# Optimization experiments

Measured on AMD Instinct MI355X. Metric: run time of the kernel, lower is better.

Reference implementation:

```python
import jax, jax.numpy as jnp
import numpy as np

N_ATOMS = 100000
N_EDGES = 1600000
N_FRAGS = 10000
N_FRAG_EDGES = 80000
D = 128


def setup_inputs() -> dict:
    key = jax.random.key(0)
    ks = jax.random.split(key, 16)
    s = 1.0 / np.sqrt(D)
    return {
        "x_atoms": jax.random.normal(ks[0], (N_ATOMS, D), jnp.float32),
        "edge_index": jax.random.randint(ks[1], (2, N_EDGES), 0, N_ATOMS),
        "edge_attr": jax.random.normal(ks[2], (N_EDGES, D), jnp.float32),
        "frag_index": jax.random.randint(ks[3], (2, N_FRAG_EDGES), 0, N_FRAGS),
        "x_frags": jax.random.normal(ks[4], (N_FRAGS, D), jnp.float32),
        "atom_to_frag_ids": jax.random.randint(ks[5], (N_ATOMS,), 0, N_FRAGS),
        # parameters (stored [in, out]); only layers actually used in forward
        "atom_w": jax.random.uniform(ks[6], (D, D), jnp.float32, -s, s),
        "atom_b": jax.random.uniform(ks[7], (D,), jnp.float32, -s, s),
        "edge_w": jax.random.uniform(ks[8], (D, D), jnp.float32, -s, s),
        "edge_b": jax.random.uniform(ks[9], (D,), jnp.float32, -s, s),
        "frag_w1": jax.random.uniform(ks[10], (D, 2 * D), jnp.float32, -s, s),
        "frag_b1": jax.random.uniform(ks[11], (2 * D,), jnp.float32, -s, s),
        "frag_w2": jax.random.uniform(ks[12], (2 * D, D), jnp.float32, -(1.0 / np.sqrt(2 * D)), 1.0 / np.sqrt(2 * D)),
        "frag_b2": jax.random.uniform(ks[13], (D,), jnp.float32, -(1.0 / np.sqrt(2 * D)), 1.0 / np.sqrt(2 * D)),
    }


def reference(x_atoms, edge_index, edge_attr, frag_index, x_frags,
              atom_to_frag_ids, atom_w, atom_b, edge_w, edge_b,
              frag_w1, frag_b1, frag_w2, frag_b2):
    n = x_atoms.shape[0]
    n_frags = x_frags.shape[0]

    # add self loops
    loop = jnp.arange(n, dtype=edge_index.dtype)
    src = jnp.concatenate([edge_index[0], loop])
    tgt = jnp.concatenate([edge_index[1], loop])
    self_loop_attr = jnp.zeros((n, edge_attr.shape[1]), edge_attr.dtype)
    edge_attr_full = jnp.concatenate([edge_attr, self_loop_attr], axis=0)

    # embeddings
    h = x_atoms @ atom_w + atom_b                      # [N, D]
    _e = edge_attr_full @ edge_w + edge_b              # computed but unused (as in source)

    # symmetric degree normalization over source-node degree
    deg = jax.ops.segment_sum(jnp.ones_like(src, dtype=h.dtype), src, num_segments=n)
    dinv = jnp.where(deg > 0, deg ** -0.5, 0.0)
    norm = dinv[src] * dinv[tgt]                       # [E+N]

    # gather - scale - scatter_add
    msg = h[src] * norm[:, None]                       # [E+N, D]
    x_atoms_new = jax.ops.segment_sum(msg, tgt, num_segments=n)

    # pool atoms into fragments
    frag_feats = jax.ops.segment_sum(x_atoms_new, atom_to_frag_ids, num_segments=n_frags)

    # fragment-level message passing
    fsrc, ftgt = frag_index[0], frag_index[1]
    frag_sum = jax.ops.segment_sum(frag_feats[fsrc], ftgt, num_segments=n_frags)

    # frag_mlp: Linear(D, 2D) -> ReLU -> Linear(2D, D)
    x_frags_new = jax.nn.relu(frag_sum @ frag_w1 + frag_b1) @ frag_w2 + frag_b2
    return (x_atoms_new, x_frags_new)
```

## Files before the change

### kernel.cpp

```cpp
#include <hip/hip_runtime.h>

constexpr int DD = 128;

typedef __attribute__((ext_vector_type(8))) short short8_t;
typedef __attribute__((ext_vector_type(8))) unsigned short ushort8_t;
typedef __attribute__((ext_vector_type(4))) float f32x4;

__device__ __forceinline__ float bf2f(unsigned short u) {
  union { unsigned int i; float f; } c;
  c.i = ((unsigned int)u) << 16;
  return c.f;
}
__device__ __forceinline__ unsigned short f2bf(float f) {
  union { float f; unsigned int i; } c;
  c.f = f;
  unsigned int x = c.i;
  x += 0x7fff + ((x >> 16) & 1);
  return (unsigned short)(x >> 16);
}

__global__ void __launch_bounds__(256) counts_gemm_k(
    const int* __restrict__ esrc, const int* __restrict__ etgt, int E,
    const int* __restrict__ a2f, int N, const int* __restrict__ ftgt, int FE,
    int* __restrict__ cnt_src, int* __restrict__ cnt_tgt,
    int* __restrict__ cnt_a2f, int* __restrict__ cnt_fe,
    int* __restrict__ rank_tgt, int* __restrict__ rank_a2f, int* __restrict__ rank_fe,
    const float* __restrict__ x, const float* __restrict__ W,
    const float* __restrict__ bias, unsigned short* __restrict__ hout,
    int nb_gemm) {
  __shared__ unsigned int wt[8192];

  if ((int)blockIdx.x >= nb_gemm) {
    int i = ((int)blockIdx.x - nb_gemm) * 256 + threadIdx.x;
    if (i < E) {
      atomicAdd(&cnt_src[esrc[i]], 1);
      rank_tgt[i] = atomicAdd(&cnt_tgt[etgt[i]], 1);
    } else if (i < E + N) {
      int j = i - E;
      rank_a2f[j] = atomicAdd(&cnt_a2f[a2f[j]], 1);
    } else if (i < E + N + FE) {
      int e = i - E - N;
      rank_fe[e] = atomicAdd(&cnt_fe[ftgt[e]], 1);
    }
    return;
  }

  const int tid = threadIdx.x;
  const int rbase = blockIdx.x * 128;

  {
    int c = tid & 127;
    int half = tid >> 7;
#pragma unroll 4
    for (int j = 0; j < 32; j++) {
      int p = j * 2 + half;
      int k = p * 2;
      float w0 = W[k * 128 + c];
      float w1 = W[(k + 1) * 128 + c];
      unsigned int packed = (unsigned int)f2bf(w0) | ((unsigned int)f2bf(w1) << 16);
      wt[(64 * c + p) ^ ((c & 7) << 2)] = packed;
    }
  }

  const int wave = tid >> 6;
  const int lane = tid & 63;
  const int l15 = lane & 15;
  const int kg = lane >> 4;

  float bcol[8];
#pragma unroll
  for (int ct = 0; ct < 8; ct++) bcol[ct] = bias[ct * 16 + l15];

  __syncthreads();

  f32x4 acc[2][8];
#pragma unroll
  for (int rt = 0; rt < 2; rt++)
#pragma unroll
    for (int ct = 0; ct < 8; ct++) acc[rt][ct] = (f32x4)(0.f);

#pragma unroll
  for (int ks = 0; ks < 4; ks++) {
    int kcol = ks * 32 + kg * 8;
    short8_t a[2];
#pragma unroll
    for (int rt = 0; rt < 2; rt++) {
      int row = rbase + wave * 32 + rt * 16 + l15;
      if (row < N) {
        const float4* xr = reinterpret_cast<const float4*>(x + (size_t)row * 128 + kcol);
        float4 v0 = xr[0], v1 = xr[1];
        a[rt][0] = (short)f2bf(v0.x); a[rt][1] = (short)f2bf(v0.y);
        a[rt][2] = (short)f2bf(v0.z); a[rt][3] = (short)f2bf(v0.w);
        a[rt][4] = (short)f2bf(v1.x); a[rt][5] = (short)f2bf(v1.y);
        a[rt][6] = (short)f2bf(v1.z); a[rt][7] = (short)f2bf(v1.w);
      } else {
#pragma unroll
        for (int e = 0; e < 8; e++) a[rt][e] = 0;
      }
    }
#pragma unroll
    for (int ct = 0; ct < 8; ct++) {
      int col = ct * 16 + l15;
      int dw0 = (64 * col + ks * 16 + kg * 4) ^ ((col & 7) << 2);
      short8_t b = *reinterpret_cast<const short8_t*>(&wt[dw0]);
      acc[0][ct] = __builtin_amdgcn_mfma_f32_16x16x32_bf16(a[0], b, acc[0][ct], 0, 0, 0);
      acc[1][ct] = __builtin_amdgcn_mfma_f32_16x16x32_bf16(a[1], b, acc[1][ct], 0, 0, 0);
    }
  }

#pragma unroll
  for (int rt = 0; rt < 2; rt++)
#pragma unroll
    for (int ct = 0; ct < 8; ct++)
#pragma unroll
      for (int i = 0; i < 4; i++) {
        int gr = rbase + wave * 32 + rt * 16 + kg * 4 + i;
        if (gr < N)
          hout[(size_t)gr * 128 + ct * 16 + l15] = f2bf(acc[rt][ct][i] + bcol[ct]);
      }
}

template<int IC, int OC, bool RELU, int RPT>
__global__ void __launch_bounds__(256) linear_k(
    const float* __restrict__ in, const float* __restrict__ W,
    const float* __restrict__ bias, float* __restrict__ out, int nrows) {
  constexpr int GROUPS = 256 / OC;
  constexpr int RBLK = RPT * GROUPS;
  __shared__ float xs[RBLK * IC];
  const int tid = threadIdx.x;
  const int c = tid % OC;
  const int g = tid / OC;
  const int rbase = blockIdx.x * RBLK;

  constexpr int NV = RBLK * IC / 4;
  const float4* in4 = reinterpret_cast<const float4*>(in);
  for (int idx = tid; idx < NV; idx += 256) {
    int r = idx / (IC / 4);
    int kk = idx % (IC / 4);
    int gr = rbase + r;
    float4 v = make_float4(0.f, 0.f, 0.f, 0.f);
    if (gr < nrows) v = in4[(size_t)gr * (IC / 4) + kk];
    reinterpret_cast<float4*>(xs)[idx] = v;
  }
  __syncthreads();

  float acc[RPT];
  float b = bias[c];
#pragma unroll
  for (int m = 0; m < RPT; m++) acc[m] = b;

#pragma unroll 4
  for (int k = 0; k < IC; k++) {
    float w = W[k * OC + c];
#pragma unroll
    for (int m = 0; m < RPT; m++)
      acc[m] += xs[(g + m * GROUPS) * IC + k] * w;
  }

#pragma unroll
  for (int m = 0; m < RPT; m++) {
    int gr = rbase + g + m * GROUPS;
    if (gr < nrows) {
      float v = acc[m];
      if (RELU) v = fmaxf(v, 0.f);
      out[(size_t)gr * OC + c] = v;
    }
  }
}

__global__ void __launch_bounds__(256) scanA_k(
    const int* __restrict__ cnt_tgt, int n, int nb, int* __restrict__ bsums,
    const int* __restrict__ cnt_a2f, int* __restrict__ off_a2f,
    const int* __restrict__ cnt_fe, int* __restrict__ off_fe, int nf) {
  __shared__ int s[256];
  int t = threadIdx.x;
  int bid = blockIdx.x;
  if (bid < nb) {
    int base = bid * 1024;
    int v = 0;
    for (int i = t; i < 1024; i += 256) {
      int g = base + i;
      if (g < n) v += cnt_tgt[g];
    }
    s[t] = v;
    __syncthreads();
    for (int d = 128; d > 0; d >>= 1) {
      if (t < d) s[t] += s[t + d];
      __syncthreads();
    }
    if (t == 0) bsums[bid] = s[0];
  } else {
    const int* in = (bid == nb) ? cnt_a2f : cnt_fe;
    int* off = (bid == nb) ? off_a2f : off_fe;
    int carry = 0;
    for (int base = 0; base < nf; base += 256) {
      int v = (base + t < nf) ? in[base + t] : 0;
      __syncthreads();
      s[t] = v;
      __syncthreads();
      for (int d = 1; d < 256; d <<= 1) {
        int u = (t >= d) ? s[t - d] : 0;
        __syncthreads();
        s[t] += u;
        __syncthreads();
      }
      if (base + t < nf) off[base + t] = s[t] - v + carry;
      carry += s[255];
    }
  }
}

__global__ void __launch_bounds__(256) scanB_k(
    const int* __restrict__ in, int n, const int* __restrict__ bsums,
    int* __restrict__ off, const int* __restrict__ cnt_src,
    float* __restrict__ dinv) {
  __shared__ int s[256];
  int t = threadIdx.x;
  int bid = blockIdx.x;
  s[t] = (t < bid) ? bsums[t] : 0;
  __syncthreads();
  for (int d = 128; d > 0; d >>= 1) {
    if (t < d) s[t] += s[t + d];
    __syncthreads();
  }
  int prefix = s[0];
  __syncthreads();

  int base = bid * 1024 + t * 4;
  int a0 = (base + 0 < n) ? in[base + 0] : 0;
  int a1 = (base + 1 < n) ? in[base + 1] : 0;
  int a2 = (base + 2 < n) ? in[base + 2] : 0;
  int a3 = (base + 3 < n) ? in[base + 3] : 0;
  int tot = a0 + a1 + a2 + a3;
  s[t] = tot;
  __syncthreads();
  for (int d = 1; d < 256; d <<= 1) {
    int u = (t >= d) ? s[t - d] : 0;
    __syncthreads();
    s[t] += u;
    __syncthreads();
  }
  int pre = s[t] - tot + prefix;
  int e0 = pre, e1 = pre + a0, e2 = e1 + a1, e3 = e2 + a2;
  if (base + 0 < n) { off[base + 0] = e0; dinv[base + 0] = rsqrtf((float)(cnt_src[base + 0] + 1)); }
  if (base + 1 < n) { off[base + 1] = e1; dinv[base + 1] = rsqrtf((float)(cnt_src[base + 1] + 1)); }
  if (base + 2 < n) { off[base + 2] = e2; dinv[base + 2] = rsqrtf((float)(cnt_src[base + 2] + 1)); }
  if (base + 3 < n) { off[base + 3] = e3; dinv[base + 3] = rsqrtf((float)(cnt_src[base + 3] + 1)); }
}

__global__ void __launch_bounds__(256) fill_k(
    const int* __restrict__ esrc, const int* __restrict__ etgt, int E,
    const int* __restrict__ a2f, int N,
    const int* __restrict__ fsrc, const int* __restrict__ ftgt, int FE,
    const int* __restrict__ off_tgt, const int* __restrict__ rank_tgt,
    const int* __restrict__ off_a2f, const int* __restrict__ rank_a2f,
    const int* __restrict__ off_fe, const int* __restrict__ rank_fe,
    int* __restrict__ csr_src, int* __restrict__ aids, int* __restrict__ csr_fs) {
  int i = blockIdx.x * 256 + threadIdx.x;
  if (i < E) {
    csr_src[off_tgt[etgt[i]] + rank_tgt[i]] = esrc[i];
  } else if (i < E + N) {
    int j = i - E;
    aids[off_a2f[a2f[j]] + rank_a2f[j]] = j;
  } else if (i < E + N + FE) {
    int e = i - E - N;
    csr_fs[off_fe[ftgt[e]] + rank_fe[e]] = fsrc[e];
  }
}

__global__ void __launch_bounds__(256) edge_gather_k(
    const int* __restrict__ off, const int* __restrict__ cnt,
    const int* __restrict__ csr_src, const unsigned short* __restrict__ h,
    const float* __restrict__ dinv, float* __restrict__ out, int n) {
  int tn = blockIdx.x * 16 + (threadIdx.x >> 4);
  if (tn >= n) return;
  int lane = threadIdx.x & 15;
  const ushort8_t* h8 = reinterpret_cast<const ushort8_t*>(h);
  float dt = dinv[tn];
  ushort8_t hv = h8[(size_t)tn * 16 + lane];
  float acc[8];
#pragma unroll
  for (int e = 0; e < 8; e++) acc[e] = bf2f(hv[e]) * dt;
  int s0 = off[tn], c = cnt[tn];
  int i = 0;
  for (; i + 4 <= c; i += 4) {
    int s1 = csr_src[s0 + i + 0];
    int s2 = csr_src[s0 + i + 1];
    int s3 = csr_src[s0 + i + 2];
    int s4 = csr_src[s0 + i + 3];
    float d1 = dinv[s1], d2 = dinv[s2], d3 = dinv[s3], d4 = dinv[s4];
    ushort8_t v1 = h8[(size_t)s1 * 16 + lane];
    ushort8_t v2 = h8[(size_t)s2 * 16 + lane];
    ushort8_t v3 = h8[(size_t)s3 * 16 + lane];
    ushort8_t v4 = h8[(size_t)s4 * 16 + lane];
#pragma unroll
    for (int e = 0; e < 8; e++)
      acc[e] += (bf2f(v1[e]) * d1 + bf2f(v2[e]) * d2) +
                (bf2f(v3[e]) * d3 + bf2f(v4[e]) * d4);
  }
  for (; i < c; i++) {
    int s1 = csr_src[s0 + i];
    float d1 = dinv[s1];
    ushort8_t v1 = h8[(size_t)s1 * 16 + lane];
#pragma unroll
    for (int e = 0; e < 8; e++) acc[e] += bf2f(v1[e]) * d1;
  }
  float4* o4 = reinterpret_cast<float4*>(out) + (size_t)tn * 32 + lane * 2;
  o4[0] = make_float4(acc[0] * dt, acc[1] * dt, acc[2] * dt, acc[3] * dt);
  o4[1] = make_float4(acc[4] * dt, acc[5] * dt, acc[6] * dt, acc[7] * dt);
}

__global__ void __launch_bounds__(256) seg_gather_k(
    const int* __restrict__ off, const int* __restrict__ cnt,
    const int* __restrict__ ids, const float* __restrict__ src_rows,
    float* __restrict__ dst, int n) {
  int f = blockIdx.x * 8 + (threadIdx.x >> 5);
  if (f >= n) return;
  int lane = threadIdx.x & 31;
  const float4* s4 = reinterpret_cast<const float4*>(src_rows);
  float ax = 0.f, ay = 0.f, az = 0.f, aw = 0.f;
  int s0 = off[f], c = cnt[f];
  int i = 0;
  for (; i + 2 <= c; i += 2) {
    int a1 = ids[s0 + i], a2 = ids[s0 + i + 1];
    float4 v1 = s4[(size_t)a1 * 32 + lane];
    float4 v2 = s4[(size_t)a2 * 32 + lane];
    ax += v1.x + v2.x; ay += v1.y + v2.y; az += v1.z + v2.z; aw += v1.w + v2.w;
  }
  if (i < c) {
    int a1 = ids[s0 + i];
    float4 v1 = s4[(size_t)a1 * 32 + lane];
    ax += v1.x; ay += v1.y; az += v1.z; aw += v1.w;
  }
  reinterpret_cast<float4*>(dst)[(size_t)f * 32 + lane] = make_float4(ax, ay, az, aw);
}

extern "C" void kernel_launch(void* const* d_in, const int* in_sizes, int n_in,
                              void* d_out, int out_size, void* d_ws, size_t ws_size,
                              hipStream_t stream) {
  const float* x_atoms    = (const float*)d_in[0];
  const int*   edge_index = (const int*)d_in[1];
  const int*   frag_index = (const int*)d_in[3];
  const int*   a2f     = (const int*)d_in[5];
  const float* atom_w  = (const float*)d_in[6];
  const float* atom_b  = (const float*)d_in[7];
  const float* frag_w1 = (const float*)d_in[10];
  const float* frag_b1 = (const float*)d_in[11];
  const float* frag_w2 = (const float*)d_in[12];
  const float* frag_b2 = (const float*)d_in[13];

  const int N  = in_sizes[0] / DD;
  const int E  = in_sizes[1] / 2;
  const int FE = in_sizes[3] / 2;
  const int NF = in_sizes[4] / DD;

  const int* esrc = edge_index;
  const int* etgt = edge_index + E;
  const int* fsrc = frag_index;
  const int* ftgt = frag_index + FE;

  float* out_atoms = (float*)d_out;
  float* out_frags = out_atoms + (size_t)N * DD;

  char* ws = (char*)d_ws;
  size_t off_b = 0;
  auto alloc = [&](size_t bytes) {
    void* p = ws + off_b;
    off_b += (bytes + 255) & ~(size_t)255;
    return p;
  };
  unsigned short* h = (unsigned short*)alloc((size_t)N * DD * 2);
  float* dinv     = (float*)alloc((size_t)N * 4);
  int*   cnts     = (int*)alloc(((size_t)2 * N + 2 * NF) * 4);
  int*   cnt_src  = cnts;
  int*   cnt_tgt  = cnts + N;
  int*   cnt_a2f  = cnts + 2 * N;
  int*   cnt_fe   = cnts + 2 * N + NF;
  int*   off_tgt  = (int*)alloc((size_t)N * 4);
  int*   rank_tgt = (int*)alloc((size_t)E * 4);
  int*   csr_src  = (int*)alloc((size_t)E * 4);
  int*   off_a2f  = (int*)alloc((size_t)NF * 4);
  int*   rank_a2f = (int*)alloc((size_t)N * 4);
  int*   aids     = (int*)alloc((size_t)N * 4);
  int*   off_fe   = (int*)alloc((size_t)NF * 4);
  int*   rank_fe  = (int*)alloc((size_t)FE * 4);
  int*   csr_fs   = (int*)alloc((size_t)FE * 4);
  int*   bsums    = (int*)alloc(1024 * 4);
  float* ff       = (float*)alloc((size_t)NF * DD * 4);
  float* fs       = (float*)alloc((size_t)NF * DD * 4);
  float* hid      = (float*)alloc((size_t)NF * 2 * DD * 4);

  hipMemsetAsync(cnts, 0, ((size_t)2 * N + 2 * NF) * 4, stream);

  int nb_gemm = (N + 127) / 128;
  int nb_cnt = (E + N + FE + 255) / 256;
  counts_gemm_k<<<nb_gemm + nb_cnt, 256, 0, stream>>>(
      esrc, etgt, E, a2f, N, ftgt, FE,
      cnt_src, cnt_tgt, cnt_a2f, cnt_fe, rank_tgt, rank_a2f, rank_fe,
      x_atoms, atom_w, atom_b, h, nb_gemm);

  int nb1 = (N + 1023) / 1024;
  scanA_k<<<nb1 + 2, 256, 0, stream>>>(cnt_tgt, N, nb1, bsums,
                                       cnt_a2f, off_a2f, cnt_fe, off_fe, NF);
  scanB_k<<<nb1, 256, 0, stream>>>(cnt_tgt, N, bsums, off_tgt, cnt_src, dinv);

  fill_k<<<nb_cnt, 256, 0, stream>>>(
      esrc, etgt, E, a2f, N, fsrc, ftgt, FE,
      off_tgt, rank_tgt, off_a2f, rank_a2f, off_fe, rank_fe,
      csr_src, aids, csr_fs);

  edge_gather_k<<<(N + 15) / 16, 256, 0, stream>>>(off_tgt, cnt_tgt, csr_src, h, dinv, out_atoms, N);
  seg_gather_k<<<(NF + 7) / 8, 256, 0, stream>>>(off_a2f, cnt_a2f, aids, out_atoms, ff, NF);
  seg_gather_k<<<(NF + 7) / 8, 256, 0, stream>>>(off_fe, cnt_fe, csr_fs, ff, fs, NF);

  linear_k<128, 256, true, 32><<<(NF + 31) / 32, 256, 0, stream>>>(fs, frag_w1, frag_b1, hid, NF);
  linear_k<256, 128, false, 16><<<(NF + 31) / 32, 256, 0, stream>>>(hid, frag_w2, frag_b2, out_frags, NF);
}
```

Measured before the change: 397.5 us.

## Prescale h by source dinv, fuse frag MLP, split counts from GEMM

Folds the source-degree normalization into h with a scaling pass merged into the CSR fill kernel, so the edge gather no longer loads dinv per neighbor and only scales by the target dinv at the end. Fuses the two fragment linear layers into one kernel that keeps the hidden activations in shared memory, dropping the global hid buffer and one launch. Splits the combined counts and GEMM kernel into two separate launches. Rounding h to bf16 after scaling adds an extra quantization step, and the launch split removes overlap between the atomics and the GEMM.

```diff
diff --git a/kernel.cpp b/kernel.cpp
--- a/kernel.cpp
+++ b/kernel.cpp
@@ -19,31 +19,29 @@
   return (unsigned short)(x >> 16);
 }
 
-__global__ void __launch_bounds__(256) counts_gemm_k(
+__global__ void __launch_bounds__(256) counts_k(
     const int* __restrict__ esrc, const int* __restrict__ etgt, int E,
     const int* __restrict__ a2f, int N, const int* __restrict__ ftgt, int FE,
     int* __restrict__ cnt_src, int* __restrict__ cnt_tgt,
     int* __restrict__ cnt_a2f, int* __restrict__ cnt_fe,
-    int* __restrict__ rank_tgt, int* __restrict__ rank_a2f, int* __restrict__ rank_fe,
+    int* __restrict__ rank_tgt, int* __restrict__ rank_a2f, int* __restrict__ rank_fe) {
+  int i = blockIdx.x * 256 + threadIdx.x;
+  if (i < E) {
+    atomicAdd(&cnt_src[esrc[i]], 1);
+    rank_tgt[i] = atomicAdd(&cnt_tgt[etgt[i]], 1);
+  } else if (i < E + N) {
+    int j = i - E;
+    rank_a2f[j] = atomicAdd(&cnt_a2f[a2f[j]], 1);
+  } else if (i < E + N + FE) {
+    int e = i - E - N;
+    rank_fe[e] = atomicAdd(&cnt_fe[ftgt[e]], 1);
+  }
+}
+
+__global__ void __launch_bounds__(256) mfma_h_k(
     const float* __restrict__ x, const float* __restrict__ W,
-    const float* __restrict__ bias, unsigned short* __restrict__ hout,
-    int nb_gemm) {
+    const float* __restrict__ bias, unsigned short* __restrict__ hout, int nrows) {
   __shared__ unsigned int wt[8192];
-
-  if ((int)blockIdx.x >= nb_gemm) {
-    int i = ((int)blockIdx.x - nb_gemm) * 256 + threadIdx.x;
-    if (i < E) {
-      atomicAdd(&cnt_src[esrc[i]], 1);
-      rank_tgt[i] = atomicAdd(&cnt_tgt[etgt[i]], 1);
-    } else if (i < E + N) {
-      int j = i - E;
-      rank_a2f[j] = atomicAdd(&cnt_a2f[a2f[j]], 1);
-    } else if (i < E + N + FE) {
-      int e = i - E - N;
-      rank_fe[e] = atomicAdd(&cnt_fe[ftgt[e]], 1);
-    }
-    return;
-  }
 
   const int tid = threadIdx.x;
   const int rbase = blockIdx.x * 128;
@@ -86,7 +84,7 @@
 #pragma unroll
     for (int rt = 0; rt < 2; rt++) {
       int row = rbase + wave * 32 + rt * 16 + l15;
-      if (row < N) {
+      if (row < nrows) {
         const float4* xr = reinterpret_cast<const float4*>(x + (size_t)row * 128 + kcol);
         float4 v0 = xr[0], v1 = xr[1];
         a[rt][0] = (short)f2bf(v0.x); a[rt][1] = (short)f2bf(v0.y);
@@ -115,57 +113,9 @@
 #pragma unroll
       for (int i = 0; i < 4; i++) {
         int gr = rbase + wave * 32 + rt * 16 + kg * 4 + i;
-        if (gr < N)
+        if (gr < nrows)
           hout[(size_t)gr * 128 + ct * 16 + l15] = f2bf(acc[rt][ct][i] + bcol[ct]);
       }
-}
-
-template<int IC, int OC, bool RELU, int RPT>
-__global__ void __launch_bounds__(256) linear_k(
-    const float* __restrict__ in, const float* __restrict__ W,
-    const float* __restrict__ bias, float* __restrict__ out, int nrows) {
-  constexpr int GROUPS = 256 / OC;
-  constexpr int RBLK = RPT * GROUPS;
-  __shared__ float xs[RBLK * IC];
-  const int tid = threadIdx.x;
-  const int c = tid % OC;
-  const int g = tid / OC;
-  const int rbase = blockIdx.x * RBLK;
-
-  constexpr int NV = RBLK * IC / 4;
-  const float4* in4 = reinterpret_cast<const float4*>(in);
-  for (int idx = tid; idx < NV; idx += 256) {
-    int r = idx / (IC / 4);
-    int kk = idx % (IC / 4);
-    int gr = rbase + r;
-    float4 v = make_float4(0.f, 0.f, 0.f, 0.f);
-    if (gr < nrows) v = in4[(size_t)gr * (IC / 4) + kk];
-    reinterpret_cast<float4*>(xs)[idx] = v;
-  }
-  __syncthreads();
-
-  float acc[RPT];
-  float b = bias[c];
-#pragma unroll
-  for (int m = 0; m < RPT; m++) acc[m] = b;
-
-#pragma unroll 4
-  for (int k = 0; k < IC; k++) {
-    float w = W[k * OC + c];
-#pragma unroll
-    for (int m = 0; m < RPT; m++)
-      acc[m] += xs[(g + m * GROUPS) * IC + k] * w;
-  }
-
-#pragma unroll
-  for (int m = 0; m < RPT; m++) {
-    int gr = rbase + g + m * GROUPS;
-    if (gr < nrows) {
-      float v = acc[m];
-      if (RELU) v = fmaxf(v, 0.f);
-      out[(size_t)gr * OC + c] = v;
-    }
-  }
 }
 
 __global__ void __launch_bounds__(256) scanA_k(
@@ -248,14 +198,26 @@
   if (base + 3 < n) { off[base + 3] = e3; dinv[base + 3] = rsqrtf((float)(cnt_src[base + 3] + 1)); }
 }
 
-__global__ void __launch_bounds__(256) fill_k(
+__global__ void __launch_bounds__(256) fill_scale_k(
     const int* __restrict__ esrc, const int* __restrict__ etgt, int E,
     const int* __restrict__ a2f, int N,
     const int* __restrict__ fsrc, const int* __restrict__ ftgt, int FE,
     const int* __restrict__ off_tgt, const int* __restrict__ rank_tgt,
     const int* __restrict__ off_a2f, const int* __restrict__ rank_a2f,
     const int* __restrict__ off_fe, const int* __restrict__ rank_fe,
-    int* __restrict__ csr_src, int* __restrict__ aids, int* __restrict__ csr_fs) {
+    int* __restrict__ csr_src, int* __restrict__ aids, int* __restrict__ csr_fs,
+    unsigned short* __restrict__ h, const float* __restrict__ dinv, int nbf) {
+  if ((int)blockIdx.x >= nbf) {
+    int idx = ((int)blockIdx.x - nbf) * 256 + threadIdx.x;
+    if (idx < N * 16) {
+      float d = dinv[idx >> 4];
+      ushort8_t v = reinterpret_cast<ushort8_t*>(h)[idx];
+#pragma unroll
+      for (int e = 0; e < 8; e++) v[e] = f2bf(bf2f(v[e]) * d);
+      reinterpret_cast<ushort8_t*>(h)[idx] = v;
+    }
+    return;
+  }
   int i = blockIdx.x * 256 + threadIdx.x;
   if (i < E) {
     csr_src[off_tgt[etgt[i]] + rank_tgt[i]] = esrc[i];
@@ -276,11 +238,10 @@
   if (tn >= n) return;
   int lane = threadIdx.x & 15;
   const ushort8_t* h8 = reinterpret_cast<const ushort8_t*>(h);
-  float dt = dinv[tn];
   ushort8_t hv = h8[(size_t)tn * 16 + lane];
   float acc[8];
 #pragma unroll
-  for (int e = 0; e < 8; e++) acc[e] = bf2f(hv[e]) * dt;
+  for (int e = 0; e < 8; e++) acc[e] = bf2f(hv[e]);
   int s0 = off[tn], c = cnt[tn];
   int i = 0;
   for (; i + 4 <= c; i += 4) {
@@ -288,23 +249,21 @@
     int s2 = csr_src[s0 + i + 1];
     int s3 = csr_src[s0 + i + 2];
     int s4 = csr_src[s0 + i + 3];
-    float d1 = dinv[s1], d2 = dinv[s2], d3 = dinv[s3], d4 = dinv[s4];
     ushort8_t v1 = h8[(size_t)s1 * 16 + lane];
     ushort8_t v2 = h8[(size_t)s2 * 16 + lane];
     ushort8_t v3 = h8[(size_t)s3 * 16 + lane];
     ushort8_t v4 = h8[(size_t)s4 * 16 + lane];
 #pragma unroll
     for (int e = 0; e < 8; e++)
-      acc[e] += (bf2f(v1[e]) * d1 + bf2f(v2[e]) * d2) +
-                (bf2f(v3[e]) * d3 + bf2f(v4[e]) * d4);
+      acc[e] += (bf2f(v1[e]) + bf2f(v2[e])) + (bf2f(v3[e]) + bf2f(v4[e]));
   }
   for (; i < c; i++) {
     int s1 = csr_src[s0 + i];
-    float d1 = dinv[s1];
     ushort8_t v1 = h8[(size_t)s1 * 16 + lane];
 #pragma unroll
-    for (int e = 0; e < 8; e++) acc[e] += bf2f(v1[e]) * d1;
-  }
+    for (int e = 0; e < 8; e++) acc[e] += bf2f(v1[e]);
+  }
+  float dt = dinv[tn];
   float4* o4 = reinterpret_cast<float4*>(out) + (size_t)tn * 32 + lane * 2;
   o4[0] = make_float4(acc[0] * dt, acc[1] * dt, acc[2] * dt, acc[3] * dt);
   o4[1] = make_float4(acc[4] * dt, acc[5] * dt, acc[6] * dt, acc[7] * dt);
@@ -333,6 +292,62 @@
     ax += v1.x; ay += v1.y; az += v1.z; aw += v1.w;
   }
   reinterpret_cast<float4*>(dst)[(size_t)f * 32 + lane] = make_float4(ax, ay, az, aw);
+}
+
+__global__ void __launch_bounds__(256) mlp_k(
+    const float* __restrict__ fs, const float* __restrict__ W1,
+    const float* __restrict__ b1, const float* __restrict__ W2,
+    const float* __restrict__ b2, float* __restrict__ out, int nrows) {
+  __shared__ float xs[32 * 128];
+  __shared__ float hs[32 * 256];
+  const int tid = threadIdx.x;
+  const int rbase = blockIdx.x * 32;
+
+  const float4* in4 = reinterpret_cast<const float4*>(fs);
+  for (int idx = tid; idx < 32 * 32; idx += 256) {
+    int r = idx / 32, kk = idx % 32;
+    int gr = rbase + r;
+    float4 v = make_float4(0.f, 0.f, 0.f, 0.f);
+    if (gr < nrows) v = in4[(size_t)gr * 32 + kk];
+    reinterpret_cast<float4*>(xs)[idx] = v;
+  }
+  __syncthreads();
+
+  {
+    float acc[32];
+    float b = b1[tid];
+#pragma unroll
+    for (int m = 0; m < 32; m++) acc[m] = b;
+#pragma unroll 4
+    for (int k = 0; k < 128; k++) {
+      float w = W1[k * 256 + tid];
+#pragma unroll
+      for (int m = 0; m < 32; m++) acc[m] += xs[m * 128 + k] * w;
+    }
+#pragma unroll
+    for (int m = 0; m < 32; m++) hs[m * 256 + tid] = fmaxf(acc[m], 0.f);
+  }
+  __syncthreads();
+
+  {
+    const int c2 = tid & 127;
+    const int g = tid >> 7;
+    float acc[16];
+    float b = b2[c2];
+#pragma unroll
+    for (int m = 0; m < 16; m++) acc[m] = b;
+#pragma unroll 4
+    for (int k = 0; k < 256; k++) {
+      float w = W2[k * 128 + c2];
+#pragma unroll
+      for (int m = 0; m < 16; m++) acc[m] += hs[(g + m * 2) * 256 + k] * w;
+    }
+#pragma unroll
+    for (int m = 0; m < 16; m++) {
+      int gr = rbase + g + m * 2;
+      if (gr < nrows) out[(size_t)gr * 128 + c2] = acc[m];
+    }
+  }
 }
 
 extern "C" void kernel_launch(void* const* d_in, const int* in_sizes, int n_in,
@@ -388,31 +403,30 @@
   int*   bsums    = (int*)alloc(1024 * 4);
   float* ff       = (float*)alloc((size_t)NF * DD * 4);
   float* fs       = (float*)alloc((size_t)NF * DD * 4);
-  float* hid      = (float*)alloc((size_t)NF * 2 * DD * 4);
 
   hipMemsetAsync(cnts, 0, ((size_t)2 * N + 2 * NF) * 4, stream);
 
-  int nb_gemm = (N + 127) / 128;
   int nb_cnt = (E + N + FE + 255) / 256;
-  counts_gemm_k<<<nb_gemm + nb_cnt, 256, 0, stream>>>(
+  counts_k<<<nb_cnt, 256, 0, stream>>>(
       esrc, etgt, E, a2f, N, ftgt, FE,
-      cnt_src, cnt_tgt, cnt_a2f, cnt_fe, rank_tgt, rank_a2f, rank_fe,
-      x_atoms, atom_w, atom_b, h, nb_gemm);
+      cnt_src, cnt_tgt, cnt_a2f, cnt_fe, rank_tgt, rank_a2f, rank_fe);
+
+  mfma_h_k<<<(N + 127) / 128, 256, 0, stream>>>(x_atoms, atom_w, atom_b, h, N);
 
   int nb1 = (N + 1023) / 1024;
   scanA_k<<<nb1 + 2, 256, 0, stream>>>(cnt_tgt, N, nb1, bsums,
                                        cnt_a2f, off_a2f, cnt_fe, off_fe, NF);
   scanB_k<<<nb1, 256, 0, stream>>>(cnt_tgt, N, bsums, off_tgt, cnt_src, dinv);
 
-  fill_k<<<nb_cnt, 256, 0, stream>>>(
+  int nb_scale = (N * 16 + 255) / 256;
+  fill_scale_k<<<nb_cnt + nb_scale, 256, 0, stream>>>(
       esrc, etgt, E, a2f, N, fsrc, ftgt, FE,
       off_tgt, rank_tgt, off_a2f, rank_a2f, off_fe, rank_fe,
-      csr_src, aids, csr_fs);
+      csr_src, aids, csr_fs, h, dinv, nb_cnt);
 
   edge_gather_k<<<(N + 15) / 16, 256, 0, stream>>>(off_tgt, cnt_tgt, csr_src, h, dinv, out_atoms, N);
   seg_gather_k<<<(NF + 7) / 8, 256, 0, stream>>>(off_a2f, cnt_a2f, aids, out_atoms, ff, NF);
   seg_gather_k<<<(NF + 7) / 8, 256, 0, stream>>>(off_fe, cnt_fe, csr_fs, ff, fs, NF);
 
-  linear_k<128, 256, true, 32><<<(NF + 31) / 32, 256, 0, stream>>>(fs, frag_w1, frag_b1, hid, NF);
-  linear_k<256, 128, false, 16><<<(NF + 31) / 32, 256, 0, stream>>>(hid, frag_w2, frag_b2, out_frags, NF);
-}
+  mlp_k<<<(NF + 31) / 32, 256, 0, stream>>>(fs, frag_w1, frag_b1, frag_w2, frag_b2, out_frags, NF);
+}
```

After: 426.7 us. +7.3%, slower.

## Prescale h by source dinv in GEMM epilogue and narrow edge gather lanes

Applied to the files above, without the earlier changes.

Splits the fused counts+GEMM kernel so the atom GEMM runs after the degree scan. The GEMM epilogue then multiplies each h row by its dinv, which removes the per-edge dinv[src] gather from the edge aggregation. The edge gather moves from 16 lanes of ushort8 to 32 lanes of ushort4 per node, with 8 nodes per block. In exchange, the GEMM no longer overlaps with the atomic counting pass, and rounding to bf16 now happens after the scaling.

```diff
diff --git a/kernel.cpp b/kernel.cpp
--- a/kernel.cpp
+++ b/kernel.cpp
@@ -3,7 +3,6 @@
 constexpr int DD = 128;
 
 typedef __attribute__((ext_vector_type(8))) short short8_t;
-typedef __attribute__((ext_vector_type(8))) unsigned short ushort8_t;
 typedef __attribute__((ext_vector_type(4))) float f32x4;
 
 __device__ __forceinline__ float bf2f(unsigned short u) {
@@ -19,31 +18,30 @@
   return (unsigned short)(x >> 16);
 }
 
-__global__ void __launch_bounds__(256) counts_gemm_k(
+__global__ void __launch_bounds__(256) counts_k(
     const int* __restrict__ esrc, const int* __restrict__ etgt, int E,
     const int* __restrict__ a2f, int N, const int* __restrict__ ftgt, int FE,
     int* __restrict__ cnt_src, int* __restrict__ cnt_tgt,
     int* __restrict__ cnt_a2f, int* __restrict__ cnt_fe,
-    int* __restrict__ rank_tgt, int* __restrict__ rank_a2f, int* __restrict__ rank_fe,
+    int* __restrict__ rank_tgt, int* __restrict__ rank_a2f, int* __restrict__ rank_fe) {
+  int i = blockIdx.x * 256 + threadIdx.x;
+  if (i < E) {
+    atomicAdd(&cnt_src[esrc[i]], 1);
+    rank_tgt[i] = atomicAdd(&cnt_tgt[etgt[i]], 1);
+  } else if (i < E + N) {
+    int j = i - E;
+    rank_a2f[j] = atomicAdd(&cnt_a2f[a2f[j]], 1);
+  } else if (i < E + N + FE) {
+    int e = i - E - N;
+    rank_fe[e] = atomicAdd(&cnt_fe[ftgt[e]], 1);
+  }
+}
+
+__global__ void __launch_bounds__(256) mfma_h_k(
     const float* __restrict__ x, const float* __restrict__ W,
-    const float* __restrict__ bias, unsigned short* __restrict__ hout,
-    int nb_gemm) {
+    const float* __restrict__ bias, const float* __restrict__ dinv,
+    unsigned short* __restrict__ hout, int nrows) {
   __shared__ unsigned int wt[8192];
-
-  if ((int)blockIdx.x >= nb_gemm) {
-    int i = ((int)blockIdx.x - nb_gemm) * 256 + threadIdx.x;
-    if (i < E) {
-      atomicAdd(&cnt_src[esrc[i]], 1);
-      rank_tgt[i] = atomicAdd(&cnt_tgt[etgt[i]], 1);
-    } else if (i < E + N) {
-      int j = i - E;
-      rank_a2f[j] = atomicAdd(&cnt_a2f[a2f[j]], 1);
-    } else if (i < E + N + FE) {
-      int e = i - E - N;
-      rank_fe[e] = atomicAdd(&cnt_fe[ftgt[e]], 1);
-    }
-    return;
-  }
 
   const int tid = threadIdx.x;
   const int rbase = blockIdx.x * 128;
@@ -70,6 +68,14 @@
   float bcol[8];
 #pragma unroll
   for (int ct = 0; ct < 8; ct++) bcol[ct] = bias[ct * 16 + l15];
+  float dv[8];
+#pragma unroll
+  for (int rt = 0; rt < 2; rt++)
+#pragma unroll
+    for (int i = 0; i < 4; i++) {
+      int gr = rbase + wave * 32 + rt * 16 + kg * 4 + i;
+      dv[rt * 4 + i] = (gr < nrows) ? dinv[gr] : 0.f;
+    }
 
   __syncthreads();
 
@@ -86,7 +92,7 @@
 #pragma unroll
     for (int rt = 0; rt < 2; rt++) {
       int row = rbase + wave * 32 + rt * 16 + l15;
-      if (row < N) {
+      if (row < nrows) {
         const float4* xr = reinterpret_cast<const float4*>(x + (size_t)row * 128 + kcol);
         float4 v0 = xr[0], v1 = xr[1];
         a[rt][0] = (short)f2bf(v0.x); a[rt][1] = (short)f2bf(v0.y);
@@ -115,8 +121,9 @@
 #pragma unroll
       for (int i = 0; i < 4; i++) {
         int gr = rbase + wave * 32 + rt * 16 + kg * 4 + i;
-        if (gr < N)
-          hout[(size_t)gr * 128 + ct * 16 + l15] = f2bf(acc[rt][ct][i] + bcol[ct]);
+        if (gr < nrows)
+          hout[(size_t)gr * 128 + ct * 16 + l15] =
+              f2bf((acc[rt][ct][i] + bcol[ct]) * dv[rt * 4 + i]);
       }
 }
 
@@ -272,15 +279,12 @@
     const int* __restrict__ off, const int* __restrict__ cnt,
     const int* __restrict__ csr_src, const unsigned short* __restrict__ h,
     const float* __restrict__ dinv, float* __restrict__ out, int n) {
-  int tn = blockIdx.x * 16 + (threadIdx.x >> 4);
+  int tn = blockIdx.x * 8 + (threadIdx.x >> 5);
   if (tn >= n) return;
-  int lane = threadIdx.x & 15;
-  const ushort8_t* h8 = reinterpret_cast<const ushort8_t*>(h);
-  float dt = dinv[tn];
-  ushort8_t hv = h8[(size_t)tn * 16 + lane];
-  float acc[8];
-#pragma unroll
-  for (int e = 0; e < 8; e++) acc[e] = bf2f(hv[e]) * dt;
+  int lane = threadIdx.x & 31;
+  const ushort4* h4 = reinterpret_cast<const ushort4*>(h);
+  ushort4 hv = h4[(size_t)tn * 32 + lane];
+  float ax = bf2f(hv.x), ay = bf2f(hv.y), az = bf2f(hv.z), aw = bf2f(hv.w);
   int s0 = off[tn], c = cnt[tn];
   int i = 0;
   for (; i + 4 <= c; i += 4) {
@@ -288,26 +292,23 @@
     int s2 = csr_src[s0 + i + 1];
     int s3 = csr_src[s0 + i + 2];
     int s4 = csr_src[s0 + i + 3];
-    float d1 = dinv[s1], d2 = dinv[s2], d3 = dinv[s3], d4 = dinv[s4];
-    ushort8_t v1 = h8[(size_t)s1 * 16 + lane];
-    ushort8_t v2 = h8[(size_t)s2 * 16 + lane];
-    ushort8_t v3 = h8[(size_t)s3 * 16 + lane];
-    ushort8_t v4 = h8[(size_t)s4 * 16 + lane];
-#pragma unroll
-    for (int e = 0; e < 8; e++)
-      acc[e] += (bf2f(v1[e]) * d1 + bf2f(v2[e]) * d2) +
-                (bf2f(v3[e]) * d3 + bf2f(v4[e]) * d4);
+    ushort4 v1 = h4[(size_t)s1 * 32 + lane];
+    ushort4 v2 = h4[(size_t)s2 * 32 + lane];
+    ushort4 v3 = h4[(size_t)s3 * 32 + lane];
+    ushort4 v4 = h4[(size_t)s4 * 32 + lane];
+    ax += (bf2f(v1.x) + bf2f(v2.x)) + (bf2f(v3.x) + bf2f(v4.x));
+    ay += (bf2f(v1.y) + bf2f(v2.y)) + (bf2f(v3.y) + bf2f(v4.y));
+    az += (bf2f(v1.z) + bf2f(v2.z)) + (bf2f(v3.z) + bf2f(v4.z));
+    aw += (bf2f(v1.w) + bf2f(v2.w)) + (bf2f(v3.w) + bf2f(v4.w));
   }
   for (; i < c; i++) {
     int s1 = csr_src[s0 + i];
-    float d1 = dinv[s1];
-    ushort8_t v1 = h8[(size_t)s1 * 16 + lane];
-#pragma unroll
-    for (int e = 0; e < 8; e++) acc[e] += bf2f(v1[e]) * d1;
-  }
-  float4* o4 = reinterpret_cast<float4*>(out) + (size_t)tn * 32 + lane * 2;
-  o4[0] = make_float4(acc[0] * dt, acc[1] * dt, acc[2] * dt, acc[3] * dt);
-  o4[1] = make_float4(acc[4] * dt, acc[5] * dt, acc[6] * dt, acc[7] * dt);
+    ushort4 v1 = h4[(size_t)s1 * 32 + lane];
+    ax += bf2f(v1.x); ay += bf2f(v1.y); az += bf2f(v1.z); aw += bf2f(v1.w);
+  }
+  float dt = dinv[tn];
+  reinterpret_cast<float4*>(out)[(size_t)tn * 32 + lane] =
+      make_float4(ax * dt, ay * dt, az * dt, aw * dt);
 }
 
 __global__ void __launch_bounds__(256) seg_gather_k(
@@ -392,24 +393,24 @@
 
   hipMemsetAsync(cnts, 0, ((size_t)2 * N + 2 * NF) * 4, stream);
 
-  int nb_gemm = (N + 127) / 128;
   int nb_cnt = (E + N + FE + 255) / 256;
-  counts_gemm_k<<<nb_gemm + nb_cnt, 256, 0, stream>>>(
+  counts_k<<<nb_cnt, 256, 0, stream>>>(
       esrc, etgt, E, a2f, N, ftgt, FE,
-      cnt_src, cnt_tgt, cnt_a2f, cnt_fe, rank_tgt, rank_a2f, rank_fe,
-      x_atoms, atom_w, atom_b, h, nb_gemm);
+      cnt_src, cnt_tgt, cnt_a2f, cnt_fe, rank_tgt, rank_a2f, rank_fe);
 
   int nb1 = (N + 1023) / 1024;
   scanA_k<<<nb1 + 2, 256, 0, stream>>>(cnt_tgt, N, nb1, bsums,
                                        cnt_a2f, off_a2f, cnt_fe, off_fe, NF);
   scanB_k<<<nb1, 256, 0, stream>>>(cnt_tgt, N, bsums, off_tgt, cnt_src, dinv);
 
+  mfma_h_k<<<(N + 127) / 128, 256, 0, stream>>>(x_atoms, atom_w, atom_b, dinv, h, N);
+
   fill_k<<<nb_cnt, 256, 0, stream>>>(
       esrc, etgt, E, a2f, N, fsrc, ftgt, FE,
       off_tgt, rank_tgt, off_a2f, rank_a2f, off_fe, rank_fe,
       csr_src, aids, csr_fs);
 
-  edge_gather_k<<<(N + 15) / 16, 256, 0, stream>>>(off_tgt, cnt_tgt, csr_src, h, dinv, out_atoms, N);
+  edge_gather_k<<<(N + 7) / 8, 256, 0, stream>>>(off_tgt, cnt_tgt, csr_src, h, dinv, out_atoms, N);
   seg_gather_k<<<(NF + 7) / 8, 256, 0, stream>>>(off_a2f, cnt_a2f, aids, out_atoms, ff, NF);
   seg_gather_k<<<(NF + 7) / 8, 256, 0, stream>>>(off_fe, cnt_fe, csr_fs, ff, fs, NF);
 
```

Result: slower. 416.6 us (+4.8%).
